# Kernel tuning notes

Hardware: AMD Instinct MI355X
Metric: run time of the kernel (lower is better)

The kernel has to match this reference:

```python
import jax, jax.numpy as jnp
import numpy as np
import math

B, CK, CV, O, T, H, W = 2, 64, 512, 2, 16, 30, 54


def setup_inputs() -> dict:
    key = jax.random.key(0)
    k1, k2, k3, k4, k5 = jax.random.split(key, 5)
    return {
        'query_key': jax.random.normal(k1, (B, CK, H, W), jnp.float32),
        'query_selection': jax.random.uniform(k2, (B, CK, H, W), jnp.float32),
        'memory_key': jax.random.normal(k3, (B, CK, T, H, W), jnp.float32),
        'memory_shrinkage': jax.random.uniform(k4, (B, 1, T, H, W), jnp.float32),
        'memory_value': jax.random.normal(k5, (B, O, CV, T, H, W), jnp.float32),
    }


def reference(query_key, query_selection, memory_key, memory_shrinkage, memory_value):
    b, ck, h, w = query_key.shape
    t = memory_key.shape[2]
    n = t * h * w          # memory bank size
    hw = h * w             # query size
    o, cv = memory_value.shape[1], memory_value.shape[2]

    mk = memory_key.reshape(b, ck, n)             # B CK N
    ms = memory_shrinkage.reshape(b, 1, n)        # B 1 N
    qk = query_key.reshape(b, ck, hw)             # B CK HW
    qe = query_selection.reshape(b, ck, hw)       # B CK HW

    # negative squared L2 distance, selection-weighted per channel:
    # -sum_c qe_c * (mk_c - qk_c)^2 = -a_sq + 2ab - b_sq
    a_sq = jnp.einsum('bcn,bcq->bnq', mk * mk, qe)          # B N HW
    two_ab = 2.0 * jnp.einsum('bcn,bcq->bnq', mk, qk * qe)  # B N HW
    b_sq = jnp.sum(qe * qk * qk, axis=1, keepdims=True)     # B 1 HW
    similarity = (-a_sq + two_ab - b_sq)
    # shrinkage scaling + 1/sqrt(CK)
    similarity = similarity * ms.reshape(b, n, 1) * (1.0 / math.sqrt(ck))

    # softmax over the memory axis N
    affinity = jax.nn.softmax(similarity, axis=1)           # B N HW

    # weighted readout
    mv = memory_value.reshape(b, o * cv, n)                 # B (O*CV) N
    mem = jnp.einsum('bvn,bnq->bvq', mv, affinity)          # B (O*CV) HW
    return mem.reshape(b, o, cv, h, w)
```

## Files before the change

kernel.cpp:

```cpp
#include <hip/hip_runtime.h>
#include <stdint.h>

#define NTOT 25920
#define OCV  1024
#define HW   1620
#define QPAD 1632
#define NBLK 810
#define KSP  8

#define MV2_STRIDE ((size_t)8 * NBLK * 4096)
#define MKP_STRIDE ((size_t)NTOT * 128)
#define QP_STRIDE  ((size_t)1664 * 128)
#define BSQ_STRIDE ((size_t)1664)
#define P_STRIDE   ((size_t)NBLK * QPAD * 32)
#define PO_STRIDE  ((size_t)KSP * OCV * QPAD)
#define LP_STRIDE  ((size_t)405 * QPAD)
#define LQ_STRIDE  ((size_t)QPAD)

typedef _Float16 f16x8 __attribute__((ext_vector_type(8)));
typedef _Float16 f16x4 __attribute__((ext_vector_type(4)));
typedef float f32x4 __attribute__((ext_vector_type(4)));
typedef float f32x16 __attribute__((ext_vector_type(16)));

__device__ __forceinline__ void gload_lds16(const void* g, void* l) {
  __builtin_amdgcn_global_load_lds(
      (const __attribute__((address_space(1))) uint32_t*)g,
      (__attribute__((address_space(3))) uint32_t*)l, 16, 0, 0);
}

__global__ __launch_bounds__(256) void k_prep_mv2(const float* __restrict__ mv,
                                                  _Float16* __restrict__ mv2,
                                                  int bBase) {
  const int nblk = blockIdx.x, vblk = blockIdx.y, bg = blockIdx.z, t = threadIdx.x;
  const float* mvb = mv + (size_t)(bBase + bg) * OCV * NTOT;
  _Float16* outb = mv2 + (size_t)bg * MV2_STRIDE + ((size_t)(vblk * NBLK + nblk)) * 4096;
  #pragma unroll
  for (int r = 0; r < 2; ++r) {
    int idx = t + r * 256;
    int row = idx >> 2, s = idx & 3, j = s ^ ((row >> 1) & 3);
    const float* src = mvb + ((size_t)(vblk * 128 + row)) * NTOT + nblk * 32 + j * 8;
    float4 a = *((const float4*)src);
    float4 c = *((const float4*)(src + 4));
    f16x8 o;
    o[0]=(_Float16)a.x; o[1]=(_Float16)a.y; o[2]=(_Float16)a.z; o[3]=(_Float16)a.w;
    o[4]=(_Float16)c.x; o[5]=(_Float16)c.y; o[6]=(_Float16)c.z; o[7]=(_Float16)c.w;
    *((f16x8*)(outb + (size_t)idx * 8)) = o;
  }
}

__global__ __launch_bounds__(256) void k_prep_mk(const float* __restrict__ mk,
                                                 _Float16* __restrict__ mkp,
                                                 int bBase) {
  __shared__ _Float16 LT[64 * 128];
  const int bg = blockIdx.y;
  const float* mkb = mk + (size_t)(bBase + bg) * 64 * NTOT;
  _Float16* mkpb = mkp + (size_t)bg * MKP_STRIDE;
  int n0 = blockIdx.x * 64;
  int c4 = threadIdx.x >> 6, nl = threadIdx.x & 63;
  for (int c = c4; c < 64; c += 4) {
    float v = mkb[(size_t)c * NTOT + n0 + nl];
    LT[nl * 128 + c]      = (_Float16)v;
    LT[nl * 128 + 64 + c] = (_Float16)(v * v);
  }
  __syncthreads();
  #pragma unroll
  for (int k = 0; k < 4; ++k) {
    int idx = threadIdx.x + 256 * k;
    int n = idx >> 4, c16 = idx & 15;
    *((uint4*)(mkpb + ((size_t)(n0 + n)) * 128 + c16 * 8)) =
        *((const uint4*)(&LT[n * 128 + c16 * 8]));
  }
}

__global__ __launch_bounds__(128) void k_prep_q(const float* __restrict__ qk,
                                                const float* __restrict__ qe,
                                                _Float16* __restrict__ qp,
                                                float* __restrict__ bsq,
                                                int bBase) {
  __shared__ _Float16 LT[128 * 128];
  const int bg = blockIdx.y;
  const float* qkb = qk + (size_t)(bBase + bg) * 64 * HW;
  const float* qeb = qe + (size_t)(bBase + bg) * 64 * HW;
  _Float16* qpb = qp + (size_t)bg * QP_STRIDE;
  int q0 = blockIdx.x * 128;
  int t = threadIdx.x;
  int q = q0 + t;
  bool valid = q < HW;
  float acc = 0.f;
  for (int c = 0; c < 64; ++c) {
    float a = valid ? qkb[(size_t)c * HW + q] : 0.f;
    float e = valid ? qeb[(size_t)c * HW + q] : 0.f;
    LT[t * 128 + c]      = (_Float16)(2.f * a * e);
    LT[t * 128 + 64 + c] = (_Float16)(-e);
    acc += e * a * a;
  }
  bsq[(size_t)bg * BSQ_STRIDE + q] = acc;
  __syncthreads();
  #pragma unroll
  for (int k = 0; k < 16; ++k) {
    int idx = t + 128 * k;
    int qq = idx >> 4, c16 = idx & 15;
    *((uint4*)(qpb + ((size_t)(q0 + qq)) * 128 + c16 * 8)) =
        *((const uint4*)(&LT[qq * 128 + c16 * 8]));
  }
}

__global__ __launch_bounds__(256) void k_S(const _Float16* __restrict__ mkp,
                                           const _Float16* __restrict__ qp,
                                           const float* __restrict__ bsq,
                                           const float* __restrict__ ms,
                                           _Float16* __restrict__ P,
                                           float* __restrict__ lpart,
                                           int bBase) {
  const int wgid = blockIdx.x;
  const int xcd = wgid & 7;
  int kk = wgid >> 3;
  const int bg = kk / 867;
  kk -= bg * 867;
  const int nloc = kk / 17, qt = kk % 17;
  const int cntn = (xcd < 5) ? 51 : 50;
  if (nloc >= cntn) return;
  const int base = (xcd < 5) ? xcd * 51 : 255 + (xcd - 5) * 50;
  const int nunit = base + nloc;
  const int n0 = nunit * 64, q0 = qt * 96;

  const _Float16* mkpb = mkp + (size_t)bg * MKP_STRIDE;
  const _Float16* qpb  = qp + (size_t)bg * QP_STRIDE;
  const float* bsqb    = bsq + (size_t)bg * BSQ_STRIDE;
  const float* msb     = ms + (size_t)(bBase + bg) * NTOT;
  _Float16* Pb         = P + (size_t)bg * P_STRIDE;
  float* lpb           = lpart + (size_t)bg * LP_STRIDE;

  const int t = threadIdx.x;
  const int w = t >> 6, l = t & 63, l15 = l & 15, g = l >> 4;
  const int ns = w >> 1, qs = w & 1;

  f16x8 qf[3][4]; float bq[3];
  #pragma unroll
  for (int qi = 0; qi < 3; ++qi) {
    int q = q0 + qs * 48 + qi * 16 + l15;
    #pragma unroll
    for (int ks = 0; ks < 4; ++ks)
      qf[qi][ks] = *((const f16x8*)(qpb + (size_t)q * 128 + (ks * 4 + g) * 8));
    bq[qi] = bsqb[q];
  }
  f16x8 af[2][4];
  #pragma unroll
  for (int nt = 0; nt < 2; ++nt) {
    int n = n0 + ns * 32 + nt * 16 + l15;
    #pragma unroll
    for (int ks = 0; ks < 4; ++ks)
      af[nt][ks] = *((const f16x8*)(mkpb + (size_t)n * 128 + (ks * 4 + g) * 8));
  }
  f32x4 sacc[2][3];
  #pragma unroll
  for (int nt = 0; nt < 2; ++nt)
    #pragma unroll
    for (int qi = 0; qi < 3; ++qi) sacc[nt][qi] = (f32x4)0.f;
  #pragma unroll
  for (int ks = 0; ks < 4; ++ks)
    #pragma unroll
    for (int nt = 0; nt < 2; ++nt)
      #pragma unroll
      for (int qi = 0; qi < 3; ++qi)
        sacc[nt][qi] = __builtin_amdgcn_mfma_f32_16x16x32_f16(af[nt][ks], qf[qi][ks], sacc[nt][qi], 0, 0, 0);

  const float K = 0.125f * 1.44269504f;
  float4 mm[2];
  #pragma unroll
  for (int nt = 0; nt < 2; ++nt)
    mm[nt] = *((const float4*)(msb + n0 + ns * 32 + nt * 16 + g * 4));
  float psum[3] = {0.f, 0.f, 0.f};
  #pragma unroll
  for (int nt = 0; nt < 2; ++nt) {
    float m0 = mm[nt].x * K, m1 = mm[nt].y * K, m2 = mm[nt].z * K, m3 = mm[nt].w * K;
    #pragma unroll
    for (int qi = 0; qi < 3; ++qi) {
      int q = q0 + qs * 48 + qi * 16 + l15;
      float bqv = bq[qi];
      float p0 = exp2f((sacc[nt][qi][0] - bqv) * m0);
      float p1 = exp2f((sacc[nt][qi][1] - bqv) * m1);
      float p2 = exp2f((sacc[nt][qi][2] - bqv) * m2);
      float p3 = exp2f((sacc[nt][qi][3] - bqv) * m3);
      psum[qi] += (p0 + p1) + (p2 + p3);
      f16x4 ph;
      ph[0]=(_Float16)p0; ph[1]=(_Float16)p1; ph[2]=(_Float16)p2; ph[3]=(_Float16)p3;
      int nblkP = nunit * 2 + ns;
      int s_lin = nt * 2 + (g >> 1);
      int s = s_lin ^ ((q >> 1) & 3);
      *((f16x4*)(Pb + ((size_t)nblkP * QPAD + q) * 32 + s * 8 + (g & 1) * 4)) = ph;
    }
  }
  #pragma unroll
  for (int qi = 0; qi < 3; ++qi) {
    psum[qi] += __shfl_xor(psum[qi], 16);
    psum[qi] += __shfl_xor(psum[qi], 32);
  }
  __shared__ float LR[2][96];
  if (g == 0) {
    #pragma unroll
    for (int qi = 0; qi < 3; ++qi) LR[ns][qs * 48 + qi * 16 + l15] = psum[qi];
  }
  __syncthreads();
  if (t < 96) lpb[(size_t)nunit * QPAD + q0 + t] = LR[0][t] + LR[1][t];
}

__global__ __launch_bounds__(256) void k_lsum(const float* __restrict__ lpart,
                                              float* __restrict__ lout) {
  const int bg = blockIdx.y;
  int q = blockIdx.x * 256 + threadIdx.x;
  if (q >= QPAD) return;
  const float* lpb = lpart + (size_t)bg * LP_STRIDE;
  float s = 0.f;
  #pragma unroll 5
  for (int i = 0; i < 405; ++i) s += lpb[(size_t)i * QPAD + q];
  lout[(size_t)bg * LQ_STRIDE + q] = s;
}

__global__ __launch_bounds__(256) void k_RO(const _Float16* __restrict__ mv2,
                                            const _Float16* __restrict__ P,
                                            _Float16* __restrict__ pO) {
  const int wgid = blockIdx.x;
  const int ksp = wgid & 7;
  int kk = wgid >> 3;
  const int bg = kk / 68;
  kk -= bg * 68;
  const int qt = kk % 17, vb2 = kk / 17;
  const int mn = (ksp < 2) ? ksp : 2;
  const int start = ksp * 101 + mn;
  const int cnt = 101 + (ksp < 2 ? 1 : 0);

  const _Float16* mv2b = mv2 + (size_t)bg * MV2_STRIDE;
  const _Float16* Pb   = P + (size_t)bg * P_STRIDE;
  _Float16* pOb        = pO + (size_t)bg * PO_STRIDE;

  const int t = threadIdx.x;
  const int w = t >> 6, l = t & 63, l31 = l & 31, kh = l >> 5;

  __shared__ _Float16 As[2][8192];
  __shared__ _Float16 Bs[2][3072];

  f32x16 acc[2][3];
  #pragma unroll
  for (int i = 0; i < 2; ++i)
    #pragma unroll
    for (int j = 0; j < 3; ++j) acc[i][j] = (f32x16)0.f;

  auto stage = [&](int nblk, int buf) {
    char* da = (char*)As[buf];
    #pragma unroll
    for (int h = 0; h < 2; ++h) {
      const char* a = (const char*)(mv2b + ((size_t)((vb2 * 2 + h) * NBLK + nblk)) * 4096);
      gload_lds16(a + t * 16, da + h * 8192 + t * 16);
      gload_lds16(a + 4096 + t * 16, da + h * 8192 + 4096 + t * 16);
    }
    const char* bsrc = (const char*)(Pb + ((size_t)nblk * QPAD + qt * 96) * 32);
    char* db = (char*)Bs[buf];
    gload_lds16(bsrc + t * 16, db + t * 16);
    if (t < 128) gload_lds16(bsrc + 4096 + t * 16, db + 4096 + t * 16);
  };

  stage(start, 0);
  asm volatile("s_waitcnt vmcnt(0)" ::: "memory");
  __builtin_amdgcn_s_barrier();
  __builtin_amdgcn_sched_barrier(0);

  for (int it = 0; it < cnt; ++it) {
    const int cur = it & 1, nxt = cur ^ 1;
    if (it + 1 < cnt) stage(start + it + 1, nxt);
    const _Float16* Ac = As[cur];
    const _Float16* Bc = Bs[cur];
    #pragma unroll
    for (int ks = 0; ks < 2; ++ks) {
      f16x8 av[2], bp[3];
      #pragma unroll
      for (int mt = 0; mt < 2; ++mt) {
        int row = w * 64 + mt * 32 + l31;
        int s = (ks * 2 + kh) ^ ((row >> 1) & 3);
        av[mt] = *((const f16x8*)(Ac + row * 32 + s * 8));
      }
      #pragma unroll
      for (int j = 0; j < 3; ++j) {
        int q = j * 32 + l31;
        int s = (ks * 2 + kh) ^ ((q >> 1) & 3);
        bp[j] = *((const f16x8*)(Bc + q * 32 + s * 8));
      }
      #pragma unroll
      for (int mt = 0; mt < 2; ++mt)
        #pragma unroll
        for (int j = 0; j < 3; ++j)
          acc[mt][j] = __builtin_amdgcn_mfma_f32_32x32x16_f16(av[mt], bp[j], acc[mt][j], 0, 0, 0);
    }
    asm volatile("s_waitcnt vmcnt(0) lgkmcnt(0)" ::: "memory");
    __builtin_amdgcn_s_barrier();
    __builtin_amdgcn_sched_barrier(0);
  }

  #pragma unroll
  for (int mt = 0; mt < 2; ++mt) {
    #pragma unroll
    for (int j = 0; j < 3; ++j) {
      int qg = qt * 96 + j * 32 + l31;
      #pragma unroll
      for (int r = 0; r < 16; ++r) {
        int rowD = (r & 3) + 8 * (r >> 2) + 4 * kh;
        int v = vb2 * 256 + w * 64 + mt * 32 + rowD;
        pOb[((size_t)ksp * OCV + v) * QPAD + qg] = (_Float16)acc[mt][j][r];
      }
    }
  }
}

__global__ __launch_bounds__(256) void k_final(const _Float16* __restrict__ pO,
                                               const float* __restrict__ lq,
                                               float* __restrict__ out,
                                               int bBase) {
  int i = blockIdx.x * 256 + threadIdx.x;
  int q = i % HW;
  int rest = i / HW;
  int v = rest & (OCV - 1);
  int bg = rest >> 10;
  const _Float16* pOb = pO + (size_t)bg * PO_STRIDE;
  float s = 0.f;
  #pragma unroll
  for (int sp = 0; sp < KSP; ++sp)
    s += (float)pOb[((size_t)sp * OCV + v) * QPAD + q];
  out[((size_t)(bBase + bg) * OCV + v) * HW + q] = s / lq[(size_t)bg * LQ_STRIDE + q];
}

static void run_batch(const float* qk, const float* qe, const float* mk,
                      const float* ms, const float* mv, float* out,
                      char* ws, int bBase, int NB, hipStream_t stream) {
  char* p = ws;
  _Float16* mv2 = (_Float16*)p; p += (size_t)NB * MV2_STRIDE * 2;
  _Float16* mkp = (_Float16*)p; p += (size_t)NB * MKP_STRIDE * 2;
  _Float16* qp  = (_Float16*)p; p += (size_t)NB * QP_STRIDE * 2;
  float* bsq    = (float*)p;    p += (size_t)NB * BSQ_STRIDE * 4;
  _Float16* P   = (_Float16*)p; p += (size_t)NB * P_STRIDE * 2;
  _Float16* pO  = (_Float16*)p; p += (size_t)NB * PO_STRIDE * 2;
  float* lpart  = (float*)p;    p += (size_t)NB * LP_STRIDE * 4;
  float* lq     = (float*)p;

  k_prep_mv2<<<dim3(NBLK, 8, NB), 256, 0, stream>>>(mv, mv2, bBase);
  k_prep_mk<<<dim3(405, NB), 256, 0, stream>>>(mk, mkp, bBase);
  k_prep_q<<<dim3(13, NB), 128, 0, stream>>>(qk, qe, qp, bsq, bBase);
  k_S<<<8 * 867 * NB, 256, 0, stream>>>(mkp, qp, bsq, ms, P, lpart, bBase);
  k_lsum<<<dim3(7, NB), 256, 0, stream>>>(lpart, lq);
  k_RO<<<8 * 68 * NB, 256, 0, stream>>>(mv2, P, pO);
  k_final<<<6480 * NB, 256, 0, stream>>>(pO, lq, out, bBase);
}

extern "C" void kernel_launch(void* const* d_in, const int* in_sizes, int n_in,
                              void* d_out, int out_size, void* d_ws, size_t ws_size,
                              hipStream_t stream) {
  const float* qk = (const float*)d_in[0];
  const float* qe = (const float*)d_in[1];
  const float* mk = (const float*)d_in[2];
  const float* ms = (const float*)d_in[3];
  const float* mv = (const float*)d_in[4];
  float* out = (float*)d_out;

  const size_t per_b = MV2_STRIDE * 2 + MKP_STRIDE * 2 + QP_STRIDE * 2 + BSQ_STRIDE * 4
                     + P_STRIDE * 2 + PO_STRIDE * 2 + LP_STRIDE * 4 + LQ_STRIDE * 4;
  if (ws_size >= 2 * per_b) {
    run_batch(qk, qe, mk, ms, mv, out, (char*)d_ws, 0, 2, stream);
  } else if (ws_size >= per_b) {
    run_batch(qk, qe, mk, ms, mv, out, (char*)d_ws, 0, 1, stream);
    run_batch(qk, qe, mk, ms, mv, out, (char*)d_ws, 1, 1, stream);
  }
}
```

Measured before the change: 592.8 us.

## Read MFMA operands directly from global memory instead of LDS staging

The value-readout GEMM kernel no longer double-buffers A and B tiles through shared memory with barriers. Each lane precomputes pointers into the pre-swizzled global layouts and loads its f16x8 fragments straight from global memory every iteration, then issues the MFMAs. This drops the LDS traffic and per-iteration barriers. In exchange it loses cross-wave data sharing, so B fragments are re-read by all four waves and there is no explicit prefetch to hide global latency.

```diff
diff --git a/kernel.cpp b/kernel.cpp
--- a/kernel.cpp
+++ b/kernel.cpp
@@ -237,8 +237,29 @@
   const int t = threadIdx.x;
   const int w = t >> 6, l = t & 63, l31 = l & 31, kh = l >> 5;
 
-  __shared__ _Float16 As[2][8192];
-  __shared__ _Float16 Bs[2][3072];
+  const char* aP[2][2];
+  #pragma unroll
+  for (int mt = 0; mt < 2; ++mt) {
+    int rloc = w * 64 + mt * 32 + l31;
+    int h = rloc >> 7, row128 = rloc & 127;
+    int vblk = vb2 * 2 + h;
+    #pragma unroll
+    for (int ks = 0; ks < 2; ++ks) {
+      int sA = (ks * 2 + kh) ^ ((row128 >> 1) & 3);
+      aP[ks][mt] = (const char*)(mv2b + ((size_t)(vblk * NBLK + start)) * 4096
+                                 + row128 * 32 + sA * 8);
+    }
+  }
+  const char* bP[2][3];
+  #pragma unroll
+  for (int j = 0; j < 3; ++j) {
+    int q = qt * 96 + j * 32 + l31;
+    #pragma unroll
+    for (int ks = 0; ks < 2; ++ks) {
+      int sB = (ks * 2 + kh) ^ ((q >> 1) & 3);
+      bP[ks][j] = (const char*)(Pb + ((size_t)start * QPAD + q) * 32 + sB * 8);
+    }
+  }
 
   f32x16 acc[2][3];
   #pragma unroll
@@ -246,54 +267,29 @@
     #pragma unroll
     for (int j = 0; j < 3; ++j) acc[i][j] = (f32x16)0.f;
 
-  auto stage = [&](int nblk, int buf) {
-    char* da = (char*)As[buf];
-    #pragma unroll
-    for (int h = 0; h < 2; ++h) {
-      const char* a = (const char*)(mv2b + ((size_t)((vb2 * 2 + h) * NBLK + nblk)) * 4096);
-      gload_lds16(a + t * 16, da + h * 8192 + t * 16);
-      gload_lds16(a + 4096 + t * 16, da + h * 8192 + 4096 + t * 16);
-    }
-    const char* bsrc = (const char*)(Pb + ((size_t)nblk * QPAD + qt * 96) * 32);
-    char* db = (char*)Bs[buf];
-    gload_lds16(bsrc + t * 16, db + t * 16);
-    if (t < 128) gload_lds16(bsrc + 4096 + t * 16, db + 4096 + t * 16);
-  };
-
-  stage(start, 0);
-  asm volatile("s_waitcnt vmcnt(0)" ::: "memory");
-  __builtin_amdgcn_s_barrier();
-  __builtin_amdgcn_sched_barrier(0);
+  const size_t strideA = 8192;
+  const size_t strideB = (size_t)QPAD * 64;
 
   for (int it = 0; it < cnt; ++it) {
-    const int cur = it & 1, nxt = cur ^ 1;
-    if (it + 1 < cnt) stage(start + it + 1, nxt);
-    const _Float16* Ac = As[cur];
-    const _Float16* Bc = Bs[cur];
+    const size_t oA = (size_t)it * strideA;
+    const size_t oB = (size_t)it * strideB;
+    f16x8 av[2][2], bp[2][3];
     #pragma unroll
     for (int ks = 0; ks < 2; ++ks) {
-      f16x8 av[2], bp[3];
-      #pragma unroll
-      for (int mt = 0; mt < 2; ++mt) {
-        int row = w * 64 + mt * 32 + l31;
-        int s = (ks * 2 + kh) ^ ((row >> 1) & 3);
-        av[mt] = *((const f16x8*)(Ac + row * 32 + s * 8));
-      }
-      #pragma unroll
-      for (int j = 0; j < 3; ++j) {
-        int q = j * 32 + l31;
-        int s = (ks * 2 + kh) ^ ((q >> 1) & 3);
-        bp[j] = *((const f16x8*)(Bc + q * 32 + s * 8));
-      }
+      #pragma unroll
+      for (int mt = 0; mt < 2; ++mt)
+        av[ks][mt] = *((const f16x8*)(aP[ks][mt] + oA));
+      #pragma unroll
+      for (int j = 0; j < 3; ++j)
+        bp[ks][j] = *((const f16x8*)(bP[ks][j] + oB));
+    }
+    #pragma unroll
+    for (int ks = 0; ks < 2; ++ks)
       #pragma unroll
       for (int mt = 0; mt < 2; ++mt)
         #pragma unroll
         for (int j = 0; j < 3; ++j)
-          acc[mt][j] = __builtin_amdgcn_mfma_f32_32x32x16_f16(av[mt], bp[j], acc[mt][j], 0, 0, 0);
-    }
-    asm volatile("s_waitcnt vmcnt(0) lgkmcnt(0)" ::: "memory");
-    __builtin_amdgcn_s_barrier();
-    __builtin_amdgcn_sched_barrier(0);
+          acc[mt][j] = __builtin_amdgcn_mfma_f32_32x32x16_f16(av[ks][mt], bp[ks][j], acc[mt][j], 0, 0, 0);
   }
 
   #pragma unroll
```

Result: slower. 605.2 us (+2.1%).
